# Kernel optimization log

Hardware: AMD Instinct MI355X
Metric: run time of the kernel (lower is better)

The kernel has to match this reference:

```python
import jax, jax.numpy as jnp
import numpy as np

N = 100000   # nodes
G = 256      # graphs
E = 120000   # edges per relation
IN = 162
HID = 128
R = 5
L = 2        # extra RGCN layers beyond the initial one


def setup_inputs() -> dict:
    key = jax.random.key(0)
    ks = jax.random.split(key, 24)
    s = 0.05
    inp = {
        "X": jax.random.normal(ks[0], (N, IN), jnp.float32),
        "batch": jnp.sort(jax.random.randint(ks[6], (N,), 0, G)),
    }
    for i in range(R):
        inp[f"edge_index{i+1}"] = jax.random.randint(ks[1 + i], (2, E), 0, N)
    # RGCN initial layer params
    inp["W0"] = jax.random.normal(ks[7], (R, IN, HID), jnp.float32) * s
    inp["root0"] = jax.random.normal(ks[8], (IN, HID), jnp.float32) * s
    inp["b0"] = jnp.zeros((HID,), jnp.float32)
    # stacked params for the L hidden RGCN layers
    inp["Wl"] = jax.random.normal(ks[9], (L, R, HID, HID), jnp.float32) * s
    inp["rootl"] = jax.random.normal(ks[10], (L, HID, HID), jnp.float32) * s
    inp["bl"] = jnp.zeros((L, HID), jnp.float32)
    # classification head
    inp["Wc1"] = jax.random.normal(ks[11], (HID, HID), jnp.float32) * s
    inp["bc1"] = jnp.zeros((HID,), jnp.float32)
    inp["Wc2"] = jax.random.normal(ks[12], (HID, HID), jnp.float32) * s
    inp["bc2"] = jnp.zeros((HID,), jnp.float32)
    inp["Wc3"] = jax.random.normal(ks[13], (HID, 1), jnp.float32) * s
    inp["bc3"] = jnp.zeros((1,), jnp.float32)
    return inp


def _seg_mean(msg, dst, num):
    # scatter-mean over destination nodes (PyG RGCNConv uses aggr='mean' per relation)
    s = jax.ops.segment_sum(msg, dst, num_segments=num)
    c = jax.ops.segment_sum(jnp.ones(msg.shape[0], msg.dtype), dst, num_segments=num)
    return s / jnp.maximum(c, 1.0)[:, None]


def _rgcn(x, W, root, b, src, dst):
    # src, dst: [R, E]; W: [R, d_in, d_out]
    msgs = jnp.einsum("ref,rfh->reh", x[src], W)          # [R, E, HID]
    agg = jax.vmap(_seg_mean, in_axes=(0, 0, None))(msgs, dst, N)  # [R, N, HID]
    return x @ root + b + agg.sum(0)


def reference(X, edge_index1, edge_index2, edge_index3, edge_index4, edge_index5,
              batch, W0, root0, b0, Wl, rootl, bl, Wc1, bc1, Wc2, bc2, Wc3, bc3):
    ei = jnp.stack([edge_index1, edge_index2, edge_index3, edge_index4, edge_index5])  # [R,2,E]
    src, dst = ei[:, 0, :], ei[:, 1, :]
    h = jax.nn.relu(_rgcn(X, W0, root0, b0, src, dst))
    for l in range(L):
        h = jax.nn.relu(_rgcn(h, Wl[l], rootl[l], bl[l], src, dst))
    # mean readout over graphs
    s = jax.ops.segment_sum(h, batch, num_segments=G)
    c = jax.ops.segment_sum(jnp.ones((N,), h.dtype), batch, num_segments=G)
    read = s / jnp.maximum(c, 1.0)[:, None]
    h = jax.nn.relu(read @ Wc1 + bc1)
    h = jax.nn.relu(h @ Wc2 + bc2)
    return h @ Wc3 + bc3
```

## Files before the change

### kernel.cpp

```cpp
#include <hip/hip_runtime.h>

#define N_NODES 100000
#define NPAD    100096
#define NTILES  782
#define TPX     98
#define G_GRAPHS 256
#define IN_F 162
#define KPAD0 192
#define HID 128
#define R_REL 5
#define L_LAYERS 2
#define M5 (R_REL * N_NODES)

typedef __attribute__((ext_vector_type(8))) short bf16x8;
typedef __attribute__((ext_vector_type(4))) float f32x4;

__device__ __forceinline__ short f2bf(float f) {
    union { float f; unsigned u; } v; v.f = f;
    unsigned r = (v.u + 0x7fffu + ((v.u >> 16) & 1u)) >> 16;
    return (short)r;
}
__device__ __forceinline__ float bf2f(unsigned short u) {
    union { unsigned u; float f; } v; v.u = ((unsigned)u) << 16;
    return v.f;
}

__global__ void k_count(const int* e0, const int* e1, const int* e2,
                        const int* e3, const int* e4, int* cnt, int E) {
    int gid = blockIdx.x * 256 + threadIdx.x;
    if (gid >= R_REL * E) return;
    int r = gid / E, e = gid - r * E;
    const int* ei = (r == 0) ? e0 : (r == 1) ? e1 : (r == 2) ? e2 : (r == 3) ? e3 : e4;
    atomicAdd(&cnt[r * N_NODES + ei[E + e]], 1);
}

__global__ __launch_bounds__(256) void k_scan1(const int* __restrict__ cnt,
                                               int* __restrict__ off, int* __restrict__ bsum) {
    __shared__ int ts[256];
    int t = threadIdx.x;
    int base = blockIdx.x * 1024 + t * 4;
    int v[4];
    #pragma unroll
    for (int j = 0; j < 4; j++) {
        int d = base + j;
        int s = 0;
        if (d < N_NODES) {
            #pragma unroll
            for (int r = 0; r < R_REL; r++) s += cnt[r * N_NODES + d];
        }
        v[j] = s;
    }
    int tsum = v[0] + v[1] + v[2] + v[3];
    ts[t] = tsum; __syncthreads();
    for (int o = 1; o < 256; o <<= 1) {
        int x = (t >= o) ? ts[t - o] : 0;
        __syncthreads();
        ts[t] += x;
        __syncthreads();
    }
    if (t == 255) bsum[blockIdx.x] = ts[255];
    int run = ts[t] - tsum;
    #pragma unroll
    for (int j = 0; j < 4; j++) { if (base + j < N_NODES) off[base + j] = run; run += v[j]; }
}

__global__ __launch_bounds__(512) void k_scan2(int* bsum, int nblk) {
    __shared__ int ts[512];
    int t = threadIdx.x;
    int v = (t < nblk) ? bsum[t] : 0;
    ts[t] = v; __syncthreads();
    for (int o = 1; o < 512; o <<= 1) {
        int x = (t >= o) ? ts[t - o] : 0;
        __syncthreads();
        ts[t] += x;
        __syncthreads();
    }
    if (t < nblk) bsum[t] = ts[t] - v;
}

__global__ void k_scan3(const int* __restrict__ off, const int* __restrict__ bsum,
                        int* __restrict__ mstart, int* __restrict__ mcur,
                        const int* __restrict__ cnt, float* __restrict__ invc) {
    int i = blockIdx.x * 256 + threadIdx.x;
    if (i >= N_NODES) return;
    int o = off[i] + bsum[i >> 10];
    mstart[i] = o;
    mcur[i] = o;
    int tc = 0;
    #pragma unroll
    for (int r = 0; r < R_REL; r++) {
        int c = cnt[r * N_NODES + i];
        tc += c;
        invc[r * N_NODES + i] = 1.0f / (float)max(c, 1);
    }
    if (i == N_NODES - 1) mstart[N_NODES] = o + tc;
}

__global__ void k_fill(const int* e0, const int* e1, const int* e2,
                       const int* e3, const int* e4, int* mcur,
                       const float* __restrict__ invc,
                       int* __restrict__ mrec, float* __restrict__ mw, int E) {
    int gid = blockIdx.x * 256 + threadIdx.x;
    if (gid >= R_REL * E) return;
    int r = gid / E, e = gid - r * E;
    const int* ei = (r == 0) ? e0 : (r == 1) ? e1 : (r == 2) ? e2 : (r == 3) ? e3 : e4;
    int src = ei[e], dst = ei[E + e];
    int pos = atomicAdd(&mcur[dst], 1);
    mrec[pos] = ((1 + r) * NPAD + src) * HID;
    mw[pos] = invc[r * N_NODES + dst];
}

__global__ void k_castX(const float* __restrict__ X, unsigned short* __restrict__ Xb) {
    int gid = blockIdx.x * 256 + threadIdx.x;
    if (gid >= NPAD * KPAD0) return;
    int row = gid / KPAD0, k = gid - row * KPAD0;
    float v = (row < N_NODES && k < IN_F) ? X[(size_t)row * IN_F + k] : 0.f;
    Xb[gid] = (unsigned short)f2bf(v);
}

__global__ void k_tw0(const float* __restrict__ root0, const float* __restrict__ W0,
                      short* __restrict__ out) {
    int gid = blockIdx.x * 256 + threadIdx.x;
    if (gid >= 6 * 128 * KPAD0) return;
    int chunk = gid / (128 * KPAD0);
    int rem = gid - chunk * 128 * KPAD0;
    int col = rem / KPAD0;
    int k = rem - col * KPAD0;
    float v = 0.f;
    if (k < IN_F)
        v = (chunk == 0) ? root0[k * HID + col]
                         : W0[((size_t)(chunk - 1) * IN_F + k) * HID + col];
    out[gid] = f2bf(v);
}

__global__ void k_twl(const float* __restrict__ rootl, const float* __restrict__ Wl,
                      short* __restrict__ out) {
    int gid = blockIdx.x * 256 + threadIdx.x;
    if (gid >= L_LAYERS * 6 * 128 * HID) return;
    int l = gid / (6 * 128 * HID);
    int rem = gid - l * 6 * 128 * HID;
    int chunk = rem / (128 * HID);
    int rem2 = rem - chunk * 128 * HID;
    int col = rem2 / HID;
    int k = rem2 - col * HID;
    float v = (chunk == 0) ? rootl[((size_t)l * HID + k) * HID + col]
                           : Wl[(((size_t)l * R_REL + (chunk - 1)) * HID + k) * HID + col];
    out[gid] = f2bf(v);
}

template<int KP>
__global__ __launch_bounds__(256)
void gemm_direct(const unsigned short* __restrict__ A, const short* __restrict__ Wt,
                 unsigned short* __restrict__ Y) {
    constexpr int KS = KP / 32;
    constexpr int PF = (KS > 4) ? 2 : KS;
    constexpr int SA = KP + 8;
    __shared__ short Bs[128 * SA];

    int bid = blockIdx.x;
    int xcd = bid & 7, slot = bid >> 3;
    int chunk = slot / TPX;
    int rt = xcd * TPX + (slot - chunk * TPX);
    if (rt >= NTILES) return;
    const int row0 = rt * 128;

    const int tid = threadIdx.x;
    const int lane = tid & 63, wv = tid >> 6;
    const int quad = lane >> 4, l16 = lane & 15;
    const int wr0 = (wv >> 1) * 64, wc0 = (wv & 1) * 64;

    const size_t arow = (size_t)(row0 + wr0 + l16) * KP + quad * 8;

    bf16x8 cur[PF][4], nxt[PF][4];
    #pragma unroll
    for (int p = 0; p < PF; p++)
        #pragma unroll
        for (int i = 0; i < 4; i++)
            cur[p][i] = *(const bf16x8*)&A[arow + (size_t)i * 16 * KP + p * 32];

    const short* Wc = Wt + (size_t)chunk * 128 * KP;
    for (int cidx = tid; cidx < 128 * (KP / 8); cidx += 256) {
        int row = cidx / (KP / 8), c8 = cidx - row * (KP / 8);
        *(bf16x8*)&Bs[row * SA + c8 * 8] = *(const bf16x8*)&Wc[row * KP + c8 * 8];
    }
    __syncthreads();

    f32x4 acc[4][4];
    #pragma unroll
    for (int i = 0; i < 4; i++)
        #pragma unroll
        for (int j = 0; j < 4; j++) acc[i][j] = (f32x4){0.f, 0.f, 0.f, 0.f};

    for (int kb = 0; kb < KS; kb += PF) {
        if (kb + PF < KS) {
            #pragma unroll
            for (int p = 0; p < PF; p++)
                #pragma unroll
                for (int i = 0; i < 4; i++)
                    nxt[p][i] = *(const bf16x8*)&A[arow + (size_t)i * 16 * KP + (kb + PF + p) * 32];
        }
        #pragma unroll
        for (int p = 0; p < PF; p++) {
            int k0 = (kb + p) * 32;
            bf16x8 bfr[4];
            #pragma unroll
            for (int j = 0; j < 4; j++)
                bfr[j] = *(const bf16x8*)&Bs[(wc0 + j * 16 + l16) * SA + k0 + quad * 8];
            #pragma unroll
            for (int i = 0; i < 4; i++)
                #pragma unroll
                for (int j = 0; j < 4; j++)
                    acc[i][j] = __builtin_amdgcn_mfma_f32_16x16x32_bf16(cur[p][i], bfr[j], acc[i][j], 0, 0, 0);
        }
        #pragma unroll
        for (int p = 0; p < PF; p++)
            #pragma unroll
            for (int i = 0; i < 4; i++)
                cur[p][i] = nxt[p][i];
    }
    __syncthreads();

    #pragma unroll
    for (int i = 0; i < 4; i++)
        #pragma unroll
        for (int j = 0; j < 4; j++)
            #pragma unroll
            for (int reg = 0; reg < 4; reg++)
                Bs[(wr0 + i * 16 + quad * 4 + reg) * SA + wc0 + j * 16 + l16] =
                    f2bf(acc[i][j][reg]);
    __syncthreads();

    unsigned short* Yc = Y + (size_t)chunk * NPAD * HID + (size_t)row0 * HID;
    #pragma unroll
    for (int s = 0; s < 8; s++) {
        int row = (tid >> 4) + s * 16;
        int col = (tid & 15) * 8;
        bf16x8 v = *(const bf16x8*)&Bs[row * SA + col];
        *(bf16x8*)&Yc[(size_t)row * HID + col] = v;
    }
}

__global__ __launch_bounds__(256)
void aggregate(const unsigned short* __restrict__ Yall, const int* __restrict__ mstart,
               const int* __restrict__ mrec, const float* __restrict__ mw,
               const float* __restrict__ bias, unsigned short* __restrict__ hout) {
    int wid = (blockIdx.x * 256 + threadIdx.x) >> 6;
    int lane = threadIdx.x & 63;
    if (wid >= N_NODES) return;
    int d = wid;
    int s = mstart[d], e = mstart[d + 1];

    float2 b2 = *(const float2*)&bias[lane * 2];
    unsigned rv = *(const unsigned*)&Yall[(size_t)d * HID + lane * 2];
    float s0 = b2.x + bf2f((unsigned short)(rv & 0xffff));
    float s1 = b2.y + bf2f((unsigned short)(rv >> 16));

    for (int base = s; base < e; base += 64) {
        int m = e - base;
        int rec = 0; float w = 0.f;
        if (lane < m) { rec = mrec[base + lane]; w = mw[base + lane]; }
        int cnt = min(m, 64);
        for (int j = 0; j < cnt; j++) {
            int off = __shfl(rec, j, 64);
            float wj = __shfl(w, j, 64);
            unsigned v = *(const unsigned*)&Yall[(size_t)off + lane * 2];
            s0 += wj * bf2f((unsigned short)(v & 0xffff));
            s1 += wj * bf2f((unsigned short)(v >> 16));
        }
    }
    unsigned lo = (unsigned short)f2bf(fmaxf(s0, 0.f));
    unsigned hi = (unsigned short)f2bf(fmaxf(s1, 0.f));
    *(unsigned*)&hout[(size_t)d * HID + lane * 2] = lo | (hi << 16);
}

__global__ __launch_bounds__(128)
void k_pool(const unsigned short* __restrict__ h, const int* __restrict__ batch,
            float* __restrict__ pooled) {
    int c = threadIdx.x;
    int start = blockIdx.x * 128;
    if (start >= N_NODES) return;
    int end = min(start + 128, N_NODES);
    int g = batch[start];
    float s = 0.f;
    for (int i = start; i < end; i++) {
        int gi = batch[i];
        if (gi != g) { atomicAdd(&pooled[g * HID + c], s); s = 0.f; g = gi; }
        s += bf2f(h[(size_t)i * HID + c]);
    }
    atomicAdd(&pooled[g * HID + c], s);
}

__device__ int lower_bound_i(const int* a, int n, int v) {
    int lo = 0, hi = n;
    while (lo < hi) {
        int mid = (lo + hi) >> 1;
        if (a[mid] < v) lo = mid + 1; else hi = mid;
    }
    return lo;
}

__global__ __launch_bounds__(128)
void k_mlp(const float* __restrict__ pooled, const int* __restrict__ batch,
           const float* __restrict__ Wc1, const float* __restrict__ bc1,
           const float* __restrict__ Wc2, const float* __restrict__ bc2,
           const float* __restrict__ Wc3, const float* __restrict__ bc3,
           float* __restrict__ out) {
    int g = blockIdx.x;
    int c = threadIdx.x;
    __shared__ int range[2];
    if (c == 0) range[0] = lower_bound_i(batch, N_NODES, g);
    if (c == 1) range[1] = lower_bound_i(batch, N_NODES, g + 1);
    __syncthreads();
    float denom = fmaxf((float)(range[1] - range[0]), 1.0f);
    __shared__ float row[HID], h1[HID], h2[HID];
    row[c] = pooled[g * HID + c] / denom;
    __syncthreads();
    float acc = bc1[c];
    for (int k = 0; k < HID; k++) acc += row[k] * Wc1[k * HID + c];
    h1[c] = fmaxf(acc, 0.f);
    __syncthreads();
    acc = bc2[c];
    for (int k = 0; k < HID; k++) acc += h1[k] * Wc2[k * HID + c];
    h2[c] = fmaxf(acc, 0.f);
    __syncthreads();
    float t = h2[c] * Wc3[c];
    for (int off = 32; off > 0; off >>= 1) t += __shfl_down(t, off, 64);
    __shared__ float part[2];
    if ((c & 63) == 0) part[c >> 6] = t;
    __syncthreads();
    if (c == 0) out[g] = part[0] + part[1] + bc3[0];
}

extern "C" void kernel_launch(void* const* d_in, const int* in_sizes, int n_in,
                              void* d_out, int out_size, void* d_ws, size_t ws_size,
                              hipStream_t stream) {
    const float* X     = (const float*)d_in[0];
    const int*   batch = (const int*)d_in[1];
    const int*   e0 = (const int*)d_in[2];
    const int*   e1 = (const int*)d_in[3];
    const int*   e2 = (const int*)d_in[4];
    const int*   e3 = (const int*)d_in[5];
    const int*   e4 = (const int*)d_in[6];
    const float* W0    = (const float*)d_in[7];
    const float* root0 = (const float*)d_in[8];
    const float* b0    = (const float*)d_in[9];
    const float* Wl    = (const float*)d_in[10];
    const float* rootl = (const float*)d_in[11];
    const float* bl    = (const float*)d_in[12];
    const float* Wc1   = (const float*)d_in[13];
    const float* bc1   = (const float*)d_in[14];
    const float* Wc2   = (const float*)d_in[15];
    const float* bc2   = (const float*)d_in[16];
    const float* Wc3   = (const float*)d_in[17];
    const float* bc3   = (const float*)d_in[18];
    const int E = in_sizes[2] / 2;
    const int NE = R_REL * E;

    char* base = (char*)d_ws;
    size_t o = 0;
    auto carve = [&](size_t bytes) -> char* {
        char* p = base + o;
        o = (o + bytes + 255) & ~(size_t)255;
        return p;
    };
    unsigned short* Y    = (unsigned short*)carve((size_t)6 * NPAD * HID * 2);
    unsigned short* hA   = (unsigned short*)carve((size_t)NPAD * HID * 2);
    unsigned short* hB   = (unsigned short*)carve((size_t)NPAD * HID * 2);
    unsigned short* Xb   = (unsigned short*)carve((size_t)NPAD * KPAD0 * 2);
    int*   cnt    = (int*)carve((size_t)M5 * 4);
    float* invc   = (float*)carve((size_t)M5 * 4);
    int*   offsc  = (int*)carve((size_t)N_NODES * 4);
    int*   mstart = (int*)carve((size_t)(N_NODES + 1) * 4);
    int*   mcur   = (int*)carve((size_t)N_NODES * 4);
    int*   mrec   = (int*)carve((size_t)NE * 4);
    float* mw     = (float*)carve((size_t)NE * 4);
    int*   bsum   = (int*)carve(2048);
    float* pooled = (float*)carve((size_t)G_GRAPHS * HID * 4);
    short* Wt0    = (short*)carve((size_t)6 * 128 * KPAD0 * 2);
    short* Wtl    = (short*)carve((size_t)L_LAYERS * 6 * 128 * HID * 2);

    hipMemsetAsync(cnt, 0, (size_t)M5 * 4, stream);
    hipMemsetAsync(pooled, 0, (size_t)G_GRAPHS * HID * 4, stream);
    int eg = (NE + 255) / 256;
    k_count<<<eg, 256, 0, stream>>>(e0, e1, e2, e3, e4, cnt, E);
    int nblk = (N_NODES + 1023) / 1024;
    k_scan1<<<nblk, 256, 0, stream>>>(cnt, offsc, bsum);
    k_scan2<<<1, 512, 0, stream>>>(bsum, nblk);
    k_scan3<<<(N_NODES + 255) / 256, 256, 0, stream>>>(offsc, bsum, mstart, mcur, cnt, invc);
    k_fill<<<eg, 256, 0, stream>>>(e0, e1, e2, e3, e4, mcur, invc, mrec, mw, E);
    k_castX<<<(NPAD * KPAD0 + 255) / 256, 256, 0, stream>>>(X, Xb);
    k_tw0<<<(6 * 128 * KPAD0 + 255) / 256, 256, 0, stream>>>(root0, W0, Wt0);
    k_twl<<<(L_LAYERS * 6 * 128 * HID + 255) / 256, 256, 0, stream>>>(rootl, Wl, Wtl);

    int ggrid = 8 * TPX * 6;
    int agg_grid = (N_NODES + 3) / 4;

    gemm_direct<KPAD0><<<ggrid, 256, 0, stream>>>(Xb, Wt0, Y);
    aggregate<<<agg_grid, 256, 0, stream>>>(Y, mstart, mrec, mw, b0, hA);

    unsigned short* hin = hA; unsigned short* hout = hB;
    for (int l = 0; l < L_LAYERS; l++) {
        gemm_direct<HID><<<ggrid, 256, 0, stream>>>(hin, Wtl + (size_t)l * 6 * 128 * HID, Y);
        aggregate<<<agg_grid, 256, 0, stream>>>(Y, mstart, mrec, mw, bl + (size_t)l * HID, hout);
        unsigned short* t = hin; hin = hout; hout = t;
    }

    k_pool<<<(N_NODES + 127) / 128, 128, 0, stream>>>(hin, batch, pooled);
    k_mlp<<<G_GRAPHS, 128, 0, stream>>>(pooled, batch, Wc1, bc1, Wc2, bc2, Wc3, bc3, (float*)d_out);
}
```

Before: 692.1 us.

## Aggregate raw features per relation before GEMM and fuse bias/ReLU into concatenated-K GEMM

```diff
diff --git a/kernel.cpp b/kernel.cpp
--- a/kernel.cpp
+++ b/kernel.cpp
@@ -3,14 +3,18 @@
 #define N_NODES 100000
 #define NPAD    100096
 #define NTILES  782
-#define TPX     98
 #define G_GRAPHS 256
 #define IN_F 162
-#define KPAD0 192
 #define HID 128
 #define R_REL 5
 #define L_LAYERS 2
 #define M5 (R_REL * N_NODES)
+#define KSEG0 192
+#define PSEG0 168
+#define SZ0   (5 * PSEG0)
+#define SZ1   (5 * HID)
+#define KC0   (6 * KSEG0)
+#define KC1   (6 * HID)
 
 typedef __attribute__((ext_vector_type(8))) short bf16x8;
 typedef __attribute__((ext_vector_type(4))) float f32x4;
@@ -41,15 +45,7 @@
     int base = blockIdx.x * 1024 + t * 4;
     int v[4];
     #pragma unroll
-    for (int j = 0; j < 4; j++) {
-        int d = base + j;
-        int s = 0;
-        if (d < N_NODES) {
-            #pragma unroll
-            for (int r = 0; r < R_REL; r++) s += cnt[r * N_NODES + d];
-        }
-        v[j] = s;
-    }
+    for (int j = 0; j < 4; j++) v[j] = (base + j < M5) ? cnt[base + j] : 0;
     int tsum = v[0] + v[1] + v[2] + v[3];
     ts[t] = tsum; __syncthreads();
     for (int o = 1; o < 256; o <<= 1) {
@@ -61,7 +57,7 @@
     if (t == 255) bsum[blockIdx.x] = ts[255];
     int run = ts[t] - tsum;
     #pragma unroll
-    for (int j = 0; j < 4; j++) { if (base + j < N_NODES) off[base + j] = run; run += v[j]; }
+    for (int j = 0; j < 4; j++) { if (base + j < M5) off[base + j] = run; run += v[j]; }
 }
 
 __global__ __launch_bounds__(512) void k_scan2(int* bsum, int nblk) {
@@ -82,38 +78,31 @@
                         int* __restrict__ mstart, int* __restrict__ mcur,
                         const int* __restrict__ cnt, float* __restrict__ invc) {
     int i = blockIdx.x * 256 + threadIdx.x;
-    if (i >= N_NODES) return;
+    if (i >= M5) return;
     int o = off[i] + bsum[i >> 10];
     mstart[i] = o;
     mcur[i] = o;
-    int tc = 0;
-    #pragma unroll
-    for (int r = 0; r < R_REL; r++) {
-        int c = cnt[r * N_NODES + i];
-        tc += c;
-        invc[r * N_NODES + i] = 1.0f / (float)max(c, 1);
-    }
-    if (i == N_NODES - 1) mstart[N_NODES] = o + tc;
+    int c = cnt[i];
+    invc[i] = 1.0f / (float)max(c, 1);
+    if (i == M5 - 1) mstart[M5] = o + c;
 }
 
 __global__ void k_fill(const int* e0, const int* e1, const int* e2,
                        const int* e3, const int* e4, int* mcur,
-                       const float* __restrict__ invc,
-                       int* __restrict__ mrec, float* __restrict__ mw, int E) {
+                       int* __restrict__ mrec, int E) {
     int gid = blockIdx.x * 256 + threadIdx.x;
     if (gid >= R_REL * E) return;
     int r = gid / E, e = gid - r * E;
     const int* ei = (r == 0) ? e0 : (r == 1) ? e1 : (r == 2) ? e2 : (r == 3) ? e3 : e4;
     int src = ei[e], dst = ei[E + e];
-    int pos = atomicAdd(&mcur[dst], 1);
-    mrec[pos] = ((1 + r) * NPAD + src) * HID;
-    mw[pos] = invc[r * N_NODES + dst];
+    int pos = atomicAdd(&mcur[r * N_NODES + dst], 1);
+    mrec[pos] = src;
 }
 
 __global__ void k_castX(const float* __restrict__ X, unsigned short* __restrict__ Xb) {
     int gid = blockIdx.x * 256 + threadIdx.x;
-    if (gid >= NPAD * KPAD0) return;
-    int row = gid / KPAD0, k = gid - row * KPAD0;
+    if (gid >= NPAD * KSEG0) return;
+    int row = gid / KSEG0, k = gid - row * KSEG0;
     float v = (row < N_NODES && k < IN_F) ? X[(size_t)row * IN_F + k] : 0.f;
     Xb[gid] = (unsigned short)f2bf(v);
 }
@@ -121,11 +110,10 @@
 __global__ void k_tw0(const float* __restrict__ root0, const float* __restrict__ W0,
                       short* __restrict__ out) {
     int gid = blockIdx.x * 256 + threadIdx.x;
-    if (gid >= 6 * 128 * KPAD0) return;
-    int chunk = gid / (128 * KPAD0);
-    int rem = gid - chunk * 128 * KPAD0;
-    int col = rem / KPAD0;
-    int k = rem - col * KPAD0;
+    if (gid >= 128 * KC0) return;
+    int col = gid / KC0;
+    int kk = gid - col * KC0;
+    int chunk = kk / KSEG0, k = kk - chunk * KSEG0;
     float v = 0.f;
     if (k < IN_F)
         v = (chunk == 0) ? root0[k * HID + col]
@@ -136,54 +124,93 @@
 __global__ void k_twl(const float* __restrict__ rootl, const float* __restrict__ Wl,
                       short* __restrict__ out) {
     int gid = blockIdx.x * 256 + threadIdx.x;
-    if (gid >= L_LAYERS * 6 * 128 * HID) return;
-    int l = gid / (6 * 128 * HID);
-    int rem = gid - l * 6 * 128 * HID;
-    int chunk = rem / (128 * HID);
-    int rem2 = rem - chunk * 128 * HID;
-    int col = rem2 / HID;
-    int k = rem2 - col * HID;
+    if (gid >= L_LAYERS * 128 * KC1) return;
+    int l = gid / (128 * KC1);
+    int rem = gid - l * 128 * KC1;
+    int col = rem / KC1;
+    int kk = rem - col * KC1;
+    int chunk = kk / HID, k = kk - chunk * HID;
     float v = (chunk == 0) ? rootl[((size_t)l * HID + k) * HID + col]
                            : Wl[(((size_t)l * R_REL + (chunk - 1)) * HID + k) * HID + col];
     out[gid] = f2bf(v);
 }
 
-template<int KP>
+template<bool L0>
 __global__ __launch_bounds__(256)
-void gemm_direct(const unsigned short* __restrict__ A, const short* __restrict__ Wt,
-                 unsigned short* __restrict__ Y) {
-    constexpr int KS = KP / 32;
-    constexpr int PF = (KS > 4) ? 2 : KS;
-    constexpr int SA = KP + 8;
-    __shared__ short Bs[128 * SA];
-
-    int bid = blockIdx.x;
-    int xcd = bid & 7, slot = bid >> 3;
-    int chunk = slot / TPX;
-    int rt = xcd * TPX + (slot - chunk * TPX);
-    if (rt >= NTILES) return;
-    const int row0 = rt * 128;
-
+void aggregate_seg(const unsigned short* __restrict__ H, unsigned short* __restrict__ Z,
+                   const int* __restrict__ mstart, const int* __restrict__ mrec,
+                   const float* __restrict__ invc) {
+    constexpr int HS = L0 ? KSEG0 : HID;
+    constexpr int ZS = L0 ? SZ0 : SZ1;
+    constexpr int PS = L0 ? PSEG0 : HID;
+    int wid = (blockIdx.x * 256 + threadIdx.x) >> 6;
+    int lane = threadIdx.x & 63;
+    if (wid >= M5) return;
+    int r = wid / N_NODES;
+    int d = wid - r * N_NODES;
+    int s = mstart[wid], e = mstart[wid + 1];
+    float s0 = 0.f, s1 = 0.f, s2 = 0.f, s3 = 0.f;
+    for (int j = s; j < e; j++) {
+        int src = mrec[j];
+        const unsigned short* row = H + (size_t)src * HS;
+        unsigned v = *(const unsigned*)(row + lane * 2);
+        s0 += bf2f((unsigned short)(v & 0xffff));
+        s1 += bf2f((unsigned short)(v >> 16));
+        if constexpr (L0) {
+            if (lane < 32) {
+                unsigned v2 = *(const unsigned*)(row + 128 + lane * 2);
+                s2 += bf2f((unsigned short)(v2 & 0xffff));
+                s3 += bf2f((unsigned short)(v2 >> 16));
+            }
+        }
+    }
+    float w = invc[wid];
+    unsigned short* dst = Z + (size_t)d * ZS + (size_t)r * PS;
+    unsigned lo = (unsigned short)f2bf(s0 * w);
+    unsigned hi = (unsigned short)f2bf(s1 * w);
+    *(unsigned*)(dst + lane * 2) = lo | (hi << 16);
+    if constexpr (L0) {
+        if (lane < 20) {
+            unsigned lo2 = (unsigned short)f2bf(s2 * w);
+            unsigned hi2 = (unsigned short)f2bf(s3 * w);
+            *(unsigned*)(dst + 128 + lane * 2) = lo2 | (hi2 << 16);
+        }
+    }
+}
+
+template<int KS0, int KSZ, int PSEG, int SA0, int SZ>
+__global__ __launch_bounds__(256)
+void gemm_seg(const unsigned short* __restrict__ A0, const unsigned short* __restrict__ Z,
+              const short* __restrict__ Wt, const float* __restrict__ bias,
+              unsigned short* __restrict__ Hout) {
+    constexpr int TS = KS0 + 5 * KSZ;
+    constexpr int KCAT = TS * 32;
+    constexpr int SE = 136;
+    __shared__ short Es[128 * SE];
+
+    const int row0 = blockIdx.x * 128;
     const int tid = threadIdx.x;
     const int lane = tid & 63, wv = tid >> 6;
     const int quad = lane >> 4, l16 = lane & 15;
     const int wr0 = (wv >> 1) * 64, wc0 = (wv & 1) * 64;
 
-    const size_t arow = (size_t)(row0 + wr0 + l16) * KP + quad * 8;
-
-    bf16x8 cur[PF][4], nxt[PF][4];
-    #pragma unroll
-    for (int p = 0; p < PF; p++)
-        #pragma unroll
-        for (int i = 0; i < 4; i++)
-            cur[p][i] = *(const bf16x8*)&A[arow + (size_t)i * 16 * KP + p * 32];
-
-    const short* Wc = Wt + (size_t)chunk * 128 * KP;
-    for (int cidx = tid; cidx < 128 * (KP / 8); cidx += 256) {
-        int row = cidx / (KP / 8), c8 = cidx - row * (KP / 8);
-        *(bf16x8*)&Bs[row * SA + c8 * 8] = *(const bf16x8*)&Wc[row * KP + c8 * 8];
-    }
-    __syncthreads();
+    const unsigned short* a0p = A0 + (size_t)(row0 + wr0 + l16) * SA0 + quad * 8;
+    const unsigned short* zp  = Z  + (size_t)(row0 + wr0 + l16) * SZ  + quad * 8;
+    const short* Bp = Wt + (size_t)(wc0 + l16) * KCAT + quad * 8;
+
+    auto ldA = [&](int t, int i) -> bf16x8 {
+        if (t < KS0)
+            return *(const bf16x8*)(a0p + (size_t)i * 16 * SA0 + t * 32);
+        int sg = (t - KS0) / KSZ, k = (t - KS0) - sg * KSZ;
+        return *(const bf16x8*)(zp + (size_t)i * 16 * SZ + sg * PSEG + k * 32);
+    };
+    auto ldB = [&](int t, int j) -> bf16x8 {
+        return *(const bf16x8*)(Bp + (size_t)j * 16 * KCAT + t * 32);
+    };
+
+    bf16x8 ac[4], bc[4];
+    #pragma unroll
+    for (int i = 0; i < 4; i++) { ac[i] = ldA(0, i); bc[i] = ldB(0, i); }
 
     f32x4 acc[4][4];
     #pragma unroll
@@ -191,86 +218,44 @@
         #pragma unroll
         for (int j = 0; j < 4; j++) acc[i][j] = (f32x4){0.f, 0.f, 0.f, 0.f};
 
-    for (int kb = 0; kb < KS; kb += PF) {
-        if (kb + PF < KS) {
+    #pragma unroll
+    for (int t = 0; t < TS; t++) {
+        bf16x8 an[4], bn[4];
+        if (t + 1 < TS) {
             #pragma unroll
-            for (int p = 0; p < PF; p++)
-                #pragma unroll
-                for (int i = 0; i < 4; i++)
-                    nxt[p][i] = *(const bf16x8*)&A[arow + (size_t)i * 16 * KP + (kb + PF + p) * 32];
+            for (int i = 0; i < 4; i++) { an[i] = ldA(t + 1, i); bn[i] = ldB(t + 1, i); }
         }
         #pragma unroll
-        for (int p = 0; p < PF; p++) {
-            int k0 = (kb + p) * 32;
-            bf16x8 bfr[4];
+        for (int i = 0; i < 4; i++)
             #pragma unroll
             for (int j = 0; j < 4; j++)
-                bfr[j] = *(const bf16x8*)&Bs[(wc0 + j * 16 + l16) * SA + k0 + quad * 8];
+                acc[i][j] = __builtin_amdgcn_mfma_f32_16x16x32_bf16(ac[i], bc[j], acc[i][j], 0, 0, 0);
+        if (t + 1 < TS) {
             #pragma unroll
-            for (int i = 0; i < 4; i++)
-                #pragma unroll
-                for (int j = 0; j < 4; j++)
-                    acc[i][j] = __builtin_amdgcn_mfma_f32_16x16x32_bf16(cur[p][i], bfr[j], acc[i][j], 0, 0, 0);
+            for (int i = 0; i < 4; i++) { ac[i] = an[i]; bc[i] = bn[i]; }
         }
-        #pragma unroll
-        for (int p = 0; p < PF; p++)
-            #pragma unroll
-            for (int i = 0; i < 4; i++)
-                cur[p][i] = nxt[p][i];
-    }
-    __syncthreads();
-
+    }
+
+    float bj[4];
+    #pragma unroll
+    for (int j = 0; j < 4; j++) bj[j] = bias[wc0 + j * 16 + l16];
     #pragma unroll
     for (int i = 0; i < 4; i++)
         #pragma unroll
         for (int j = 0; j < 4; j++)
             #pragma unroll
             for (int reg = 0; reg < 4; reg++)
-                Bs[(wr0 + i * 16 + quad * 4 + reg) * SA + wc0 + j * 16 + l16] =
-                    f2bf(acc[i][j][reg]);
-    __syncthreads();
-
-    unsigned short* Yc = Y + (size_t)chunk * NPAD * HID + (size_t)row0 * HID;
+                Es[(wr0 + i * 16 + quad * 4 + reg) * SE + wc0 + j * 16 + l16] =
+                    f2bf(fmaxf(acc[i][j][reg] + bj[j], 0.f));
+    __syncthreads();
+
     #pragma unroll
     for (int s = 0; s < 8; s++) {
         int row = (tid >> 4) + s * 16;
         int col = (tid & 15) * 8;
-        bf16x8 v = *(const bf16x8*)&Bs[row * SA + col];
-        *(bf16x8*)&Yc[(size_t)row * HID + col] = v;
-    }
-}
-
-__global__ __launch_bounds__(256)
-void aggregate(const unsigned short* __restrict__ Yall, const int* __restrict__ mstart,
-               const int* __restrict__ mrec, const float* __restrict__ mw,
-               const float* __restrict__ bias, unsigned short* __restrict__ hout) {
-    int wid = (blockIdx.x * 256 + threadIdx.x) >> 6;
-    int lane = threadIdx.x & 63;
-    if (wid >= N_NODES) return;
-    int d = wid;
-    int s = mstart[d], e = mstart[d + 1];
-
-    float2 b2 = *(const float2*)&bias[lane * 2];
-    unsigned rv = *(const unsigned*)&Yall[(size_t)d * HID + lane * 2];
-    float s0 = b2.x + bf2f((unsigned short)(rv & 0xffff));
-    float s1 = b2.y + bf2f((unsigned short)(rv >> 16));
-
-    for (int base = s; base < e; base += 64) {
-        int m = e - base;
-        int rec = 0; float w = 0.f;
-        if (lane < m) { rec = mrec[base + lane]; w = mw[base + lane]; }
-        int cnt = min(m, 64);
-        for (int j = 0; j < cnt; j++) {
-            int off = __shfl(rec, j, 64);
-            float wj = __shfl(w, j, 64);
-            unsigned v = *(const unsigned*)&Yall[(size_t)off + lane * 2];
-            s0 += wj * bf2f((unsigned short)(v & 0xffff));
-            s1 += wj * bf2f((unsigned short)(v >> 16));
-        }
-    }
-    unsigned lo = (unsigned short)f2bf(fmaxf(s0, 0.f));
-    unsigned hi = (unsigned short)f2bf(fmaxf(s1, 0.f));
-    *(unsigned*)&hout[(size_t)d * HID + lane * 2] = lo | (hi << 16);
+        bf16x8 v = *(const bf16x8*)&Es[row * SE + col];
+        *(bf16x8*)&Hout[(size_t)(row0 + row) * HID + col] = v;
+    }
 }
 
 __global__ __launch_bounds__(128)
@@ -363,48 +348,49 @@
         o = (o + bytes + 255) & ~(size_t)255;
         return p;
     };
-    unsigned short* Y    = (unsigned short*)carve((size_t)6 * NPAD * HID * 2);
-    unsigned short* hA   = (unsigned short*)carve((size_t)NPAD * HID * 2);
-    unsigned short* hB   = (unsigned short*)carve((size_t)NPAD * HID * 2);
-    unsigned short* Xb   = (unsigned short*)carve((size_t)NPAD * KPAD0 * 2);
+    unsigned short* h1 = (unsigned short*)carve((size_t)NPAD * HID * 2);
+    unsigned short* Xb = (unsigned short*)carve((size_t)NPAD * KSEG0 * 2);
+    unsigned short* Z0 = (unsigned short*)carve((size_t)NPAD * SZ0 * 2 + 256);
     int*   cnt    = (int*)carve((size_t)M5 * 4);
     float* invc   = (float*)carve((size_t)M5 * 4);
-    int*   offsc  = (int*)carve((size_t)N_NODES * 4);
-    int*   mstart = (int*)carve((size_t)(N_NODES + 1) * 4);
-    int*   mcur   = (int*)carve((size_t)N_NODES * 4);
+    int*   offsc  = (int*)carve((size_t)M5 * 4);
+    int*   mstart = (int*)carve((size_t)(M5 + 1) * 4);
     int*   mrec   = (int*)carve((size_t)NE * 4);
-    float* mw     = (float*)carve((size_t)NE * 4);
     int*   bsum   = (int*)carve(2048);
     float* pooled = (float*)carve((size_t)G_GRAPHS * HID * 4);
-    short* Wt0    = (short*)carve((size_t)6 * 128 * KPAD0 * 2);
-    short* Wtl    = (short*)carve((size_t)L_LAYERS * 6 * 128 * HID * 2);
+    short* Wt0    = (short*)carve((size_t)128 * KC0 * 2);
+    short* Wtl    = (short*)carve((size_t)L_LAYERS * 128 * KC1 * 2);
+    int*   mcur   = offsc;
+    unsigned short* h2 = Xb;
+    unsigned short* Z1 = Z0;
 
     hipMemsetAsync(cnt, 0, (size_t)M5 * 4, stream);
     hipMemsetAsync(pooled, 0, (size_t)G_GRAPHS * HID * 4, stream);
+    hipMemsetAsync(Z0 + (size_t)N_NODES * SZ0, 0,
+                   ((size_t)(NPAD - N_NODES) * SZ0 + 64) * 2, stream);
     int eg = (NE + 255) / 256;
     k_count<<<eg, 256, 0, stream>>>(e0, e1, e2, e3, e4, cnt, E);
-    int nblk = (N_NODES + 1023) / 1024;
+    int nblk = (M5 + 1023) / 1024;
     k_scan1<<<nblk, 256, 0, stream>>>(cnt, offsc, bsum);
     k_scan2<<<1, 512, 0, stream>>>(bsum, nblk);
-    k_scan3<<<(N_NODES + 255) / 256, 256, 0, stream>>>(offsc, bsum, mstart, mcur, cnt, invc);
-    k_fill<<<eg, 256, 0, stream>>>(e0, e1, e2, e3, e4, mcur, invc, mrec, mw, E);
-    k_castX<<<(NPAD * KPAD0 + 255) / 256, 256, 0, stream>>>(X, Xb);
-    k_tw0<<<(6 * 128 * KPAD0 + 255) / 256, 256, 0, stream>>>(root0, W0, Wt0);
-    k_twl<<<(L_LAYERS * 6 * 128 * HID + 255) / 256, 256, 0, stream>>>(rootl, Wl, Wtl);
-
-    int ggrid = 8 * TPX * 6;
-    int agg_grid = (N_NODES + 3) / 4;
-
-    gemm_direct<KPAD0><<<ggrid, 256, 0, stream>>>(Xb, Wt0, Y);
-    aggregate<<<agg_grid, 256, 0, stream>>>(Y, mstart, mrec, mw, b0, hA);
-
-    unsigned short* hin = hA; unsigned short* hout = hB;
-    for (int l = 0; l < L_LAYERS; l++) {
-        gemm_direct<HID><<<ggrid, 256, 0, stream>>>(hin, Wtl + (size_t)l * 6 * 128 * HID, Y);
-        aggregate<<<agg_grid, 256, 0, stream>>>(Y, mstart, mrec, mw, bl + (size_t)l * HID, hout);
-        unsigned short* t = hin; hin = hout; hout = t;
-    }
-
-    k_pool<<<(N_NODES + 127) / 128, 128, 0, stream>>>(hin, batch, pooled);
+    k_scan3<<<(M5 + 255) / 256, 256, 0, stream>>>(offsc, bsum, mstart, mcur, cnt, invc);
+    k_fill<<<eg, 256, 0, stream>>>(e0, e1, e2, e3, e4, mcur, mrec, E);
+    k_castX<<<(NPAD * KSEG0 + 255) / 256, 256, 0, stream>>>(X, Xb);
+    k_tw0<<<(128 * KC0 + 255) / 256, 256, 0, stream>>>(root0, W0, Wt0);
+    k_twl<<<(L_LAYERS * 128 * KC1 + 255) / 256, 256, 0, stream>>>(rootl, Wl, Wtl);
+
+    const int agrid = (M5 * 64) / 256;
+
+    aggregate_seg<true><<<agrid, 256, 0, stream>>>(Xb, Z0, mstart, mrec, invc);
+    gemm_seg<6, 6, PSEG0, KSEG0, SZ0><<<NTILES, 256, 0, stream>>>(Xb, Z0, Wt0, b0, h1);
+
+    aggregate_seg<false><<<agrid, 256, 0, stream>>>(h1, Z1, mstart, mrec, invc);
+    gemm_seg<4, 4, HID, HID, SZ1><<<NTILES, 256, 0, stream>>>(h1, Z1, Wtl, bl, h2);
+
+    aggregate_seg<false><<<agrid, 256, 0, stream>>>(h2, Z1, mstart, mrec, invc);
+    gemm_seg<4, 4, HID, HID, SZ1><<<NTILES, 256, 0, stream>>>(h2, Z1, Wtl + (size_t)128 * KC1,
+                                                              bl + HID, h1);
+
+    k_pool<<<(N_NODES + 127) / 128, 128, 0, stream>>>(h1, batch, pooled);
     k_mlp<<<G_GRAPHS, 128, 0, stream>>>(pooled, batch, Wc1, bc1, Wc2, bc2, Wc3, bc3, (float*)d_out);
 }
```

After: 948.4 us. +37.0%, slower.
